# Kernel optimization log

Hardware: AMD Instinct MI355X
Metric: run time of the kernel (lower is better)

## Reference

```python
import jax, jax.numpy as jnp
import numpy as np

B, T, M, D, H, DK, DV = 2, 1024, 1024, 1024, 16, 64, 64
R = 2 * T + M  # number of relative positions required by rel_shift path


def setup_inputs() -> dict:
    key = jax.random.key(0)
    ks = jax.random.split(key, 11)
    s = 0.02
    return {
        "inputs": jax.random.normal(ks[0], (B, T, D), jnp.float32),
        "attention_mask": jnp.ones((B, T, M + T), jnp.float32),
        "positional_encodings": jax.random.normal(ks[1], (R, D), jnp.float32),
        "memory": jax.random.normal(ks[2], (B, M, D), jnp.float32),
        "Wq": jax.random.normal(ks[3], (D, H * DK), jnp.float32) * s,
        "Wk": jax.random.normal(ks[4], (D, H * DK), jnp.float32) * s,
        "Wv": jax.random.normal(ks[5], (D, H * DV), jnp.float32) * s,
        "Wr": jax.random.normal(ks[6], (D, H * DK), jnp.float32) * s,
        "r_w_bias": jax.random.normal(ks[7], (H, DK), jnp.float32) * s,
        "r_r_bias": jax.random.normal(ks[8], (H, DK), jnp.float32) * s,
        "W_out": jax.random.normal(ks[9], (H * DV, D), jnp.float32) * s,
    }


def _rel_shift(m, attention_length):
    # m: [T_q, T_q + L] -> [T_q, L], TXL relative shift via reshape/slice
    tq, total = m.shape
    x = m.reshape(total, tq)[1:].reshape(tq, total - 1)
    return x[:, :attention_length]


def reference(inputs, attention_mask, positional_encodings, memory,
              Wq, Wk, Wv, Wr, r_w_bias, r_r_bias, W_out):
    b, t, d = inputs.shape
    values = jnp.concatenate([memory, inputs], axis=1)  # [B, L, D]
    L = values.shape[1]
    q = (inputs @ Wq).reshape(b, t, H, DK)
    k = (values @ Wk).reshape(b, L, H, DK)
    v = (values @ Wv).reshape(b, L, H, DV)
    rk = (positional_encodings @ Wr).reshape(-1, H, DK)  # [R, H, DK]
    # content + relative logits (TXL)
    content = jnp.einsum('bthd,bThd->bhtT', q + r_w_bias, k)        # [B,H,T,L]
    rel = jnp.einsum('bthd,rhd->bhtr', q + r_r_bias, rk)            # [B,H,T,R]
    rel = jax.vmap(jax.vmap(lambda m: _rel_shift(m, L)))(rel)       # [B,H,T,L]
    logits = (content + rel) * (DK ** -0.5)
    masked = logits - (1.0 - attention_mask[:, None, :, :]) * 1e30
    w = jax.nn.softmax(masked, axis=-1)
    attn = jnp.einsum('bhtT,bThd->bthd', w, v)                      # [B,T,H,DV]
    return attn.reshape(b, t, H * DV) @ W_out
```

## Files before the change

### kernel.cpp

```cpp
#include <hip/hip_runtime.h>
#include <hip/hip_fp16.h>
#include <stdint.h>

#define Bz 2
#define Tq 1024
#define Mm 1024
#define Hh 16
#define Ll 2048
#define Rr 3072

typedef __attribute__((ext_vector_type(8))) short bf16x8;
typedef __attribute__((ext_vector_type(4))) float f32x4;

typedef __attribute__((address_space(3))) uint8_t lds_u8_t;
typedef __attribute__((address_space(1))) uint8_t glb_u8_t;

__device__ __forceinline__ void gl2lds16(const void* g, void* l) {
  __builtin_amdgcn_global_load_lds((const glb_u8_t*)g, (lds_u8_t*)l, 16, 0, 0);
}

__device__ __forceinline__ unsigned short f2bf(float f) {
  unsigned int u = __builtin_bit_cast(unsigned int, f);
  u = u + 0x7fffu + ((u >> 16) & 1u);
  return (unsigned short)(u >> 16);
}
__device__ __forceinline__ float b2f(unsigned short s) {
  unsigned int u = ((unsigned int)s) << 16;
  return __builtin_bit_cast(float, u);
}
__device__ __forceinline__ unsigned int cvt_pk_bf16(float lo, float hi) {
  unsigned int r;
  asm volatile("v_cvt_pk_bf16_f32 %0, %1, %2" : "=v"(r) : "v"(lo), "v"(hi));
  return r;
}

__global__ __launch_bounds__(256) void k_prep2(
    const float* __restrict__ x, const float* __restrict__ mem,
    const float* __restrict__ pos,
    const float* __restrict__ w0, const float* __restrict__ w1,
    const float* __restrict__ w2, const float* __restrict__ w3,
    const float* __restrict__ w4,
    unsigned short* __restrict__ vin, unsigned short* __restrict__ pb,
    unsigned short* __restrict__ t0, unsigned short* __restrict__ t1,
    unsigned short* __restrict__ t2, unsigned short* __restrict__ t3,
    unsigned short* __restrict__ t4) {
  __shared__ float tile[64][65];
  int bid = blockIdx.x;
  if (bid < 4096) {
    int idx = bid * 256 + threadIdx.x;
    int e = idx << 2;
    int row = e >> 10, col = e & 1023;
    int b = row >> 11, l = row & 2047;
    const float* s = (l < Mm) ? (mem + (((size_t)b * Mm + l) << 10) + col)
                              : (x + (((size_t)b * Tq + (l - Mm)) << 10) + col);
    float4 v = *(const float4*)s;
    ushort4 o;
    o.x = f2bf(v.x); o.y = f2bf(v.y); o.z = f2bf(v.z); o.w = f2bf(v.w);
    *(ushort4*)(vin + e) = o;
  } else if (bid < 7168) {
    int idx = (bid - 4096) * 256 + threadIdx.x;
    int e = idx << 2;
    float4 v = *(const float4*)(pos + e);
    ushort4 t;
    t.x = f2bf(v.x); t.y = f2bf(v.y); t.z = f2bf(v.z); t.w = f2bf(v.w);
    *(ushort4*)(pb + e) = t;
  } else {
    int r3 = bid - 7168;
    int mz = r3 >> 8, rem = r3 & 255;
    const float* W;
    unsigned short* WT;
    switch (mz) {
      case 0: W = w0; WT = t0; break;
      case 1: W = w1; WT = t1; break;
      case 2: W = w2; WT = t2; break;
      case 3: W = w3; WT = t3; break;
      default: W = w4; WT = t4; break;
    }
    int k0 = (rem >> 4) * 64, n0 = (rem & 15) * 64;
    int tid = threadIdx.x;
    int rr = tid >> 4, c4 = (tid & 15) * 4;
#pragma unroll
    for (int it = 0; it < 4; ++it) {
      int r = rr + it * 16;
      float4 v = *(const float4*)(W + (size_t)(k0 + r) * 1024 + n0 + c4);
      tile[r][c4] = v.x; tile[r][c4 + 1] = v.y;
      tile[r][c4 + 2] = v.z; tile[r][c4 + 3] = v.w;
    }
    __syncthreads();
#pragma unroll
    for (int it = 0; it < 4; ++it) {
      int n = rr + it * 16;
      ushort4 o;
      o.x = f2bf(tile[c4 + 0][n]); o.y = f2bf(tile[c4 + 1][n]);
      o.z = f2bf(tile[c4 + 2][n]); o.w = f2bf(tile[c4 + 3][n]);
      *(ushort4*)(WT + (size_t)(n0 + n) * 1024 + k0 + c4) = o;
    }
  }
}

template <int RMAP>
__device__ __forceinline__ void gemm_pipe(const unsigned short* __restrict__ A,
                                          const unsigned short* __restrict__ Bt,
                                          int m0, int n0, unsigned short* As,
                                          unsigned short* Bs, f32x4 acc[4][4]) {
  const int tid = threadIdx.x;
  const int w = tid >> 6, lane = tid & 63;
  const int quad = lane >> 4, li = lane & 15;
  const int wr = w >> 1, wc = w & 1;
  f32x4 z = {0.f, 0.f, 0.f, 0.f};
#pragma unroll
  for (int mi = 0; mi < 4; ++mi)
#pragma unroll
    for (int ni = 0; ni < 4; ++ni) acc[mi][ni] = z;

  const int rs = lane >> 2;
  const int cs = lane & 3;

#pragma unroll
  for (int s = 0; s < 2; ++s) {
    int i = w * 2 + s;
    int r = i * 16 + rs;
    int c = cs ^ ((r >> 1) & 3);
    int ar = m0 + r;
    if (RMAP) ar = ar + 1024 + (ar & 1024);
    gl2lds16(A + (size_t)ar * 1024 + c * 8, (char*)As + i * 1024);
    gl2lds16(Bt + (size_t)(n0 + r) * 1024 + c * 8, (char*)Bs + i * 1024);
  }

  for (int k0 = 0; k0 < 1024; k0 += 32) {
    const int bo = ((k0 >> 5) & 1) * 8192;
    const int no = bo ^ 8192;
    __builtin_amdgcn_s_waitcnt(0x0F70);
    __syncthreads();
    if (k0 + 32 < 1024) {
#pragma unroll
      for (int s = 0; s < 2; ++s) {
        int i = w * 2 + s;
        int r = i * 16 + rs;
        int c = cs ^ ((r >> 1) & 3);
        int ar = m0 + r;
        if (RMAP) ar = ar + 1024 + (ar & 1024);
        gl2lds16(A + (size_t)ar * 1024 + k0 + 32 + c * 8,
                 (char*)As + no + i * 1024);
        gl2lds16(Bt + (size_t)(n0 + r) * 1024 + k0 + 32 + c * 8,
                 (char*)Bs + no + i * 1024);
      }
    }
    bf16x8 af[4], bfr[4];
#pragma unroll
    for (int mi = 0; mi < 4; ++mi) {
      int r = wr * 64 + mi * 16 + li;
      int ch = quad ^ ((r >> 1) & 3);
      af[mi] = *(const bf16x8*)((const char*)As + bo + r * 64 + ch * 16);
    }
#pragma unroll
    for (int ni = 0; ni < 4; ++ni) {
      int r = wc * 64 + ni * 16 + li;
      int ch = quad ^ ((r >> 1) & 3);
      bfr[ni] = *(const bf16x8*)((const char*)Bs + bo + r * 64 + ch * 16);
    }
#pragma unroll
    for (int mi = 0; mi < 4; ++mi)
#pragma unroll
      for (int ni = 0; ni < 4; ++ni)
        acc[mi][ni] = __builtin_amdgcn_mfma_f32_16x16x32_bf16(
            af[mi], bfr[ni], acc[mi][ni], 0, 0, 0);
  }
}

__global__ __launch_bounds__(256) void k_proj(
    const unsigned short* __restrict__ Vin, const unsigned short* __restrict__ Pb,
    const unsigned short* __restrict__ WqT, const unsigned short* __restrict__ WkT,
    const unsigned short* __restrict__ WvT, const unsigned short* __restrict__ WrT,
    unsigned short* __restrict__ qb, unsigned short* __restrict__ kb,
    unsigned short* __restrict__ vtb, unsigned short* __restrict__ rkb) {
  __shared__ unsigned short As[2 * 128 * 32];
  __shared__ unsigned short Bs[2 * 128 * 32];
  const int t = blockIdx.x;
  const int tid = threadIdx.x, w = tid >> 6, lane = tid & 63;
  const int quad = lane >> 4, li = lane & 15, wr = w >> 1, wc = w & 1;
  f32x4 acc[4][4];

  if (t < 256) {
    int m0 = (t >> 3) * 128, n0 = (t & 7) * 128;
    gemm_pipe<0>(Vin, WkT, m0, n0, As, Bs, acc);
#pragma unroll
    for (int mi = 0; mi < 4; ++mi)
#pragma unroll
      for (int ni = 0; ni < 4; ++ni)
#pragma unroll
        for (int reg = 0; reg < 4; ++reg) {
          int rrow = m0 + wr * 64 + mi * 16 + quad * 4 + reg;
          int cc = n0 + wc * 64 + ni * 16 + li;
          kb[(size_t)rrow * 1024 + cc] = f2bf(acc[mi][ni][reg]);
        }
  } else if (t < 512) {
    int tt = t - 256;
    int m0 = (tt >> 3) * 128, n0 = (tt & 7) * 128;
    gemm_pipe<0>(Vin, WvT, m0, n0, As, Bs, acc);
    unsigned short* T = As;
    int b = m0 >> 11, l0b = m0 & 2047;
    int rr2 = tid >> 2, q2 = tid & 3;
#pragma unroll
    for (int p = 0; p < 2; ++p) {
      __syncthreads();
      if (wc == p) {
#pragma unroll
        for (int mi = 0; mi < 4; ++mi)
#pragma unroll
          for (int ni = 0; ni < 4; ++ni) {
            int ccl = ni * 16 + li;
            int ll = wr * 64 + mi * 16 + quad * 4;
            ushort4 o;
            o.x = f2bf(acc[mi][ni][0]); o.y = f2bf(acc[mi][ni][1]);
            o.z = f2bf(acc[mi][ni][2]); o.w = f2bf(acc[mi][ni][3]);
            *(ushort4*)(T + ccl * 128 + ll) = o;
          }
      }
      __syncthreads();
      const uint4* src = (const uint4*)(T + rr2 * 128 + q2 * 32);
      uint4 v0 = src[0], v1 = src[1], v2 = src[2], v3 = src[3];
      uint4* dp = (uint4*)(vtb +
          ((size_t)(b * 1024 + n0 + p * 64 + rr2)) * Ll + l0b + q2 * 32);
      dp[0] = v0; dp[1] = v1; dp[2] = v2; dp[3] = v3;
    }
  } else if (t < 640) {
    int tt = t - 512;
    int m0 = (tt >> 3) * 128, n0 = (tt & 7) * 128;
    gemm_pipe<1>(Vin, WqT, m0, n0, As, Bs, acc);
#pragma unroll
    for (int mi = 0; mi < 4; ++mi)
#pragma unroll
      for (int ni = 0; ni < 4; ++ni)
#pragma unroll
        for (int reg = 0; reg < 4; ++reg) {
          int rrow = m0 + wr * 64 + mi * 16 + quad * 4 + reg;
          int cc = n0 + wc * 64 + ni * 16 + li;
          qb[(size_t)rrow * 1024 + cc] = f2bf(acc[mi][ni][reg]);
        }
  } else {
    int tt = t - 640;
    int m0 = (tt >> 3) * 128, n0 = (tt & 7) * 128;
    gemm_pipe<0>(Pb, WrT, m0, n0, As, Bs, acc);
#pragma unroll
    for (int mi = 0; mi < 4; ++mi)
#pragma unroll
      for (int ni = 0; ni < 4; ++ni)
#pragma unroll
        for (int reg = 0; reg < 4; ++reg) {
          int rrow = m0 + wr * 64 + mi * 16 + quad * 4 + reg;
          int cc = n0 + wc * 64 + ni * 16 + li;
          rkb[(size_t)rrow * 1024 + cc] = f2bf(acc[mi][ni][reg]);
        }
  }
}

__global__ __launch_bounds__(256) void k_gemm_out64(
    const unsigned short* __restrict__ attnb, const unsigned short* __restrict__ WoT,
    float* __restrict__ out) {
  __shared__ unsigned short As[2 * 64 * 32];
  __shared__ unsigned short Bs[2 * 64 * 32];
  int m0 = blockIdx.x * 64, n0 = blockIdx.y * 64;
  const int tid = threadIdx.x, w = tid >> 6, lane = tid & 63;
  const int quad = lane >> 4, li = lane & 15, wr = w >> 1, wc = w & 1;
  f32x4 z = {0.f, 0.f, 0.f, 0.f};
  f32x4 acc[2][2];
#pragma unroll
  for (int mi = 0; mi < 2; ++mi)
#pragma unroll
    for (int ni = 0; ni < 2; ++ni) acc[mi][ni] = z;
  const int rs = lane >> 2, cs = lane & 3;

  {
    int r = w * 16 + rs;
    int c = cs ^ ((r >> 1) & 3);
    gl2lds16(attnb + (size_t)(m0 + r) * 1024 + c * 8, (char*)As + w * 1024);
    gl2lds16(WoT + (size_t)(n0 + r) * 1024 + c * 8, (char*)Bs + w * 1024);
  }

  for (int k0 = 0; k0 < 1024; k0 += 32) {
    const int bo = ((k0 >> 5) & 1) * 4096;
    __builtin_amdgcn_s_waitcnt(0x0F70);
    __syncthreads();
    if (k0 + 32 < 1024) {
      int r = w * 16 + rs;
      int c = cs ^ ((r >> 1) & 3);
      gl2lds16(attnb + (size_t)(m0 + r) * 1024 + k0 + 32 + c * 8,
               (char*)As + (bo ^ 4096) + w * 1024);
      gl2lds16(WoT + (size_t)(n0 + r) * 1024 + k0 + 32 + c * 8,
               (char*)Bs + (bo ^ 4096) + w * 1024);
    }
    bf16x8 af[2], bfr[2];
#pragma unroll
    for (int mi = 0; mi < 2; ++mi) {
      int r = wr * 32 + mi * 16 + li;
      int ch = quad ^ ((r >> 1) & 3);
      af[mi] = *(const bf16x8*)((const char*)As + bo + r * 64 + ch * 16);
    }
#pragma unroll
    for (int ni = 0; ni < 2; ++ni) {
      int r = wc * 32 + ni * 16 + li;
      int ch = quad ^ ((r >> 1) & 3);
      bfr[ni] = *(const bf16x8*)((const char*)Bs + bo + r * 64 + ch * 16);
    }
#pragma unroll
    for (int mi = 0; mi < 2; ++mi)
#pragma unroll
      for (int ni = 0; ni < 2; ++ni)
        acc[mi][ni] = __builtin_amdgcn_mfma_f32_16x16x32_bf16(
            af[mi], bfr[ni], acc[mi][ni], 0, 0, 0);
  }
#pragma unroll
  for (int mi = 0; mi < 2; ++mi)
#pragma unroll
    for (int ni = 0; ni < 2; ++ni)
#pragma unroll
      for (int reg = 0; reg < 4; ++reg) {
        int rrow = m0 + wr * 32 + mi * 16 + quad * 4 + reg;
        int cc = n0 + wc * 32 + ni * 16 + li;
        out[(size_t)rrow * 1024 + cc] = acc[mi][ni][reg];
      }
}

__global__ __launch_bounds__(512, 4) void k_attn(
    const unsigned short* __restrict__ qb, const float* __restrict__ rwb,
    const float* __restrict__ rrb,
    const unsigned short* __restrict__ kb, const unsigned short* __restrict__ vt,
    const unsigned short* __restrict__ rkb, const float* __restrict__ maskf,
    unsigned short* __restrict__ attnb) {
  __shared__ __align__(16) uint8_t lds[75776];

  const int tid = threadIdx.x;
  const int w = tid >> 6, lane = tid & 63;
  const int quad = lane >> 4, li = lane & 15;
  const int wq = w & 3, grp = w >> 2;
  const int srow = lane >> 3, scs = lane & 7;
  const int flat = blockIdx.x + 16 * blockIdx.y + 256 * blockIdx.z;
  const int qt = (flat >> 3) & 15;
  const int g = 4 * (flat & 7) + (flat >> 7);
  const int h = g & 15, b = g >> 4;
  const int t0blk = qt * 64;
  const int t0w = t0blk + wq * 16;
  const int rboff = 48 - 16 * wq;
  const int rbase0 = Tq - t0blk - 63;
  const int jbase = grp * 1024;

  unsigned short* KS = (unsigned short*)(lds + grp * 8192);
  unsigned short* VS = (unsigned short*)(lds + 16384 + grp * 8192);
  unsigned short* RS = (unsigned short*)(lds + 32768 + grp * 16384);
  unsigned short* pw = (unsigned short*)(lds + 65536 + w * 1280);
  float* red = (float*)(lds + 32768);

  const unsigned short* kbase = kb + ((size_t)(b * Ll + jbase) * Hh + h) * 64;
  const unsigned short* vbase = vt + ((size_t)((b * Hh + h) * 64)) * Ll + jbase;
  const unsigned short* rkbase = rkb + (size_t)h * 64;
  const float* mrowf = maskf + ((size_t)(b * Tq + t0w + li)) * Ll + jbase;

  bf16x8 aqw[2], aqr[2];
  {
    const unsigned short* p1 = qb + ((size_t)((b * Tq + t0w + li) * Hh + h)) * 64;
#pragma unroll
    for (int ks = 0; ks < 2; ++ks) {
      bf16x8 qf = *(const bf16x8*)(p1 + ks * 32 + quad * 8);
      const float* wp = rwb + h * 64 + ks * 32 + quad * 8;
      const float* rp = rrb + h * 64 + ks * 32 + quad * 8;
      float4 w0 = *(const float4*)wp, w1 = *(const float4*)(wp + 4);
      float4 r0 = *(const float4*)rp, r1 = *(const float4*)(rp + 4);
      float wv[8] = {w0.x, w0.y, w0.z, w0.w, w1.x, w1.y, w1.z, w1.w};
      float rv[8] = {r0.x, r0.y, r0.z, r0.w, r1.x, r1.y, r1.z, r1.w};
#pragma unroll
      for (int i2 = 0; i2 < 8; ++i2) {
        float qv = b2f((unsigned short)qf[i2]);
        aqw[ks][i2] = (short)f2bf(qv + wv[i2]);
        aqr[ks][i2] = (short)f2bf(qv + rv[i2]);
      }
    }
  }

  f32x4 z = {0.f, 0.f, 0.f, 0.f};
  f32x4 o[4];
  o[0] = z; o[1] = z; o[2] = z; o[3] = z;
  f32x4 ol = z;
  float nmf[8] = {0.f, 0.f, 0.f, 0.f, 0.f, 0.f, 0.f, 0.f};

  const float SC = 0.125f * 1.4426950408889634f;
  const float BIGM = 1.442695e30f;
  const short oneb = 0x3F80;
  const bf16x8 onesf = {oneb, oneb, oneb, oneb, oneb, oneb, oneb, oneb};

  int srcl[4];
#pragma unroll
  for (int reg = 0; reg < 4; ++reg) {
    int row = quad * 4 + reg;
    srcl[reg] = (lane & 48) + ((li + row + 1) & 15);
  }

  auto finish = [&](const unsigned short* VsP, const float (&mv)[8]) {
    bf16x8 sv = *(const bf16x8*)(pw + li * 40 + quad * 8);
    float p[8];
#pragma unroll
    for (int i2 = 0; i2 < 8; ++i2) {
      float sf = __half2float(__builtin_bit_cast(__half, (unsigned short)sv[i2]));
      float mvneg = fmaf(mv[i2], BIGM, -BIGM);
      p[i2] = exp2f(fmaf(sf, SC, mvneg));
    }
    int4 pk;
    pk.x = (int)cvt_pk_bf16(p[0], p[1]);
    pk.y = (int)cvt_pk_bf16(p[2], p[3]);
    pk.z = (int)cvt_pk_bf16(p[4], p[5]);
    pk.w = (int)cvt_pk_bf16(p[6], p[7]);
    bf16x8 apv = __builtin_bit_cast(bf16x8, pk);
    __builtin_amdgcn_s_setprio(1);
    ol = __builtin_amdgcn_mfma_f32_16x16x32_bf16(apv, onesf, ol, 0, 0, 0);
#pragma unroll
    for (int nt = 0; nt < 4; ++nt) {
      int dv = nt * 16 + li;
      int ch = quad ^ ((dv >> 1) & 3);
      bf16x8 vf = *(const bf16x8*)(VsP + dv * 32 + ch * 8);
      o[nt] = __builtin_amdgcn_mfma_f32_16x16x32_bf16(apv, vf, o[nt], 0, 0, 0);
    }
    __builtin_amdgcn_s_setprio(0);
  };

#pragma unroll
  for (int pass = 0; pass < 3; ++pass) {
    int u = pass * 32 + wq * 8 + srow;
    int gr = rbase0 + jbase + u;
    if (gr > Rr - 1) gr = Rr - 1;
    int c = scs ^ srow;
    gl2lds16(rkbase + (size_t)gr * 1024 + c * 8, RS + (pass * 32 + wq * 8) * 64);
  }
  {
    int r = wq * 8 + srow;
    int c = scs ^ srow;
    gl2lds16(kbase + (size_t)r * 1024 + c * 8, KS + wq * 512);
  }

  for (int jt = 0; jt < 32; ++jt) {
    const int jloc = jt * 32;
    __builtin_amdgcn_s_waitcnt(0x0F70);
    __syncthreads();
    if (jt < 31) {
      {
        int r = wq * 8 + srow;
        int c = scs ^ srow;
        gl2lds16(kbase + (size_t)(jloc + 32 + r) * 1024 + c * 8,
                 KS + (((jt + 1) & 1) * 2048) + wq * 512);
      }
      {
        int u = jloc + 96 + wq * 8 + srow;
        int gr = rbase0 + jbase + u;
        if (gr > Rr - 1) gr = Rr - 1;
        int c = scs ^ srow;
        gl2lds16(rkbase + (size_t)gr * 1024 + c * 8,
                 RS + ((jloc + 96 + wq * 8) & 127) * 64);
      }
    }
    {
      int dv = wq * 16 + (lane >> 2);
      int c = (lane & 3) ^ ((dv >> 1) & 3);
      gl2lds16(vbase + (size_t)dv * Ll + jloc + c * 8,
               VS + ((jt & 1) * 2048) + wq * 512);
    }
    asm volatile("" ::: "memory");
    const unsigned short* KsC = KS + (jt & 1) * 2048;
    f32x4 sc[2];
    sc[0] = z; sc[1] = z;
    __builtin_amdgcn_s_setprio(1);
#pragma unroll
    for (int ks = 0; ks < 2; ++ks)
#pragma unroll
      for (int nt = 0; nt < 2; ++nt) {
        int j = nt * 16 + li;
        int ch = (ks * 4 + quad) ^ (j & 7);
        bf16x8 kf = *(const bf16x8*)(KsC + j * 64 + ch * 8);
        sc[nt] = __builtin_amdgcn_mfma_f32_16x16x32_bf16(aqw[ks], kf, sc[nt], 0, 0, 0);
      }
    f32x4 bd[3];
    bd[0] = z; bd[1] = z; bd[2] = z;
#pragma unroll
    for (int ks = 0; ks < 2; ++ks)
#pragma unroll
      for (int nt = 0; nt < 3; ++nt) {
        int pr = (rboff + nt * 16 + li + jloc) & 127;
        int ch = (ks * 4 + quad) ^ (pr & 7);
        bf16x8 rf = *(const bf16x8*)(RS + pr * 64 + ch * 8);
        bd[nt] = __builtin_amdgcn_mfma_f32_16x16x32_bf16(aqr[ks], rf, bd[nt], 0, 0, 0);
      }
    __builtin_amdgcn_s_setprio(0);
    if (jt > 0) finish(VS + ((jt - 1) & 1) * 2048, nmf);
    {
      float4 m0 = *(const float4*)(mrowf + jloc + quad * 8);
      float4 m1 = *(const float4*)(mrowf + jloc + quad * 8 + 4);
      nmf[0] = m0.x; nmf[1] = m0.y; nmf[2] = m0.z; nmf[3] = m0.w;
      nmf[4] = m1.x; nmf[5] = m1.y; nmf[6] = m1.z; nmf[7] = m1.w;
    }
    float rot[2][4];
#pragma unroll
    for (int nt = 0; nt < 2; ++nt)
#pragma unroll
      for (int reg = 0; reg < 4; ++reg)
        rot[nt][reg] = __shfl(sc[nt][reg], srcl[reg], 64);
#pragma unroll
    for (int nt = 0; nt < 3; ++nt)
#pragma unroll
      for (int reg = 0; reg < 4; ++reg) {
        int row = quad * 4 + reg;
        int jj = nt * 16 + li + row - 15;
        int nthi = (nt > 1) ? 0 : nt;
        int ntlo = (nt == 0) ? 0 : (nt - 1);
        float val = ((li + row) >= 15) ? rot[nthi][reg] : rot[ntlo][reg];
        float s = val + bd[nt][reg];
        if ((unsigned)jj < 32u)
          pw[row * 40 + jj] = __builtin_bit_cast(unsigned short, __float2half(s));
      }
  }
  __builtin_amdgcn_s_waitcnt(0x0F70);
  __syncthreads();
  finish(VS + 2048, nmf);

  if (grp == 1) {
    float* rp = red + (size_t)(wq * 64 + lane) * 20;
#pragma unroll
    for (int nt = 0; nt < 4; ++nt)
#pragma unroll
      for (int reg = 0; reg < 4; ++reg) rp[nt * 4 + reg] = o[nt][reg];
#pragma unroll
    for (int reg = 0; reg < 4; ++reg) rp[16 + reg] = ol[reg];
  }
  __syncthreads();
  if (grp == 0) {
    const float* rp = red + (size_t)(wq * 64 + lane) * 20;
    float inv[4];
#pragma unroll
    for (int reg = 0; reg < 4; ++reg) inv[reg] = 1.0f / (ol[reg] + rp[16 + reg]);
#pragma unroll
    for (int nt = 0; nt < 4; ++nt)
#pragma unroll
      for (int reg = 0; reg < 4; ++reg) {
        int trow = t0w + quad * 4 + reg;
        float val = (o[nt][reg] + rp[nt * 4 + reg]) * inv[reg];
        attnb[((size_t)(b * Tq + trow)) * 1024 + h * 64 + nt * 16 + li] = f2bf(val);
      }
  }
}

extern "C" void kernel_launch(void* const* d_in, const int* in_sizes, int n_in,
                              void* d_out, int out_size, void* d_ws, size_t ws_size,
                              hipStream_t stream) {
  const float* x = (const float*)d_in[0];
  const float* mask = (const float*)d_in[1];
  const float* pos = (const float*)d_in[2];
  const float* mem = (const float*)d_in[3];
  const float* Wq = (const float*)d_in[4];
  const float* Wk = (const float*)d_in[5];
  const float* Wv = (const float*)d_in[6];
  const float* Wr = (const float*)d_in[7];
  const float* rwb = (const float*)d_in[8];
  const float* rrb = (const float*)d_in[9];
  const float* Wo = (const float*)d_in[10];
  float* out = (float*)d_out;

  uint8_t* ws = (uint8_t*)d_ws;
  const size_t MB = 1024 * 1024;
  unsigned short* Vinb = (unsigned short*)(ws + 0);
  unsigned short* WqT = (unsigned short*)(ws + 8 * MB);
  unsigned short* WkT = (unsigned short*)(ws + 10 * MB);
  unsigned short* WvT = (unsigned short*)(ws + 12 * MB);
  unsigned short* WrT = (unsigned short*)(ws + 14 * MB);
  unsigned short* WoT = (unsigned short*)(ws + 16 * MB);
  unsigned short* Pb = (unsigned short*)(ws + 18 * MB);
  unsigned short* qb = (unsigned short*)(ws + 24 * MB);
  unsigned short* kb = (unsigned short*)(ws + 32 * MB);
  unsigned short* vtb = (unsigned short*)(ws + 40 * MB);
  unsigned short* rkb = (unsigned short*)(ws + 48 * MB);
  unsigned short* attnb = (unsigned short*)(ws + 19 * MB);

  hipLaunchKernelGGL(k_prep2, dim3(8448), dim3(256), 0, stream,
                     x, mem, pos, Wq, Wk, Wv, Wr, Wo,
                     Vinb, Pb, WqT, WkT, WvT, WrT, WoT);
  hipLaunchKernelGGL(k_proj, dim3(832), dim3(256), 0, stream,
                     Vinb, Pb, WqT, WkT, WvT, WrT, qb, kb, vtb, rkb);
  hipLaunchKernelGGL(k_attn, dim3(16, 16, 2), dim3(512), 0, stream,
                     qb, rwb, rrb, kb, vtb, rkb, mask, attnb);
  hipLaunchKernelGGL(k_gemm_out64, dim3(32, 16), dim3(256), 0, stream,
                     attnb, WoT, out);
}
```

Before: 268.6 us.

## Remap projection tile order for XCD locality and drop LDS transpose for V

Block indices in the fused projection kernel are remapped so that consecutive blocks (likely spread round-robin across the 8 XCDs) share the same row band. This is meant to improve L2 reuse of A and B tiles. The V-projection epilogue no longer stages a transpose through LDS with two barriers. Each wave instead writes ushort4 fragments straight into the transposed layout. That removes the syncs and LDS traffic but gives narrower, more scattered global stores.

```diff
diff --git a/kernel.cpp b/kernel.cpp
--- a/kernel.cpp
+++ b/kernel.cpp
@@ -182,7 +182,8 @@
   f32x4 acc[4][4];
 
   if (t < 256) {
-    int m0 = (t >> 3) * 128, n0 = (t & 7) * 128;
+    int a = t & 7, n = (t >> 3) & 7, c = t >> 6;
+    int m0 = (4 * a + c) * 128, n0 = n * 128;
     gemm_pipe<0>(Vin, WkT, m0, n0, As, Bs, acc);
 #pragma unroll
     for (int mi = 0; mi < 4; ++mi)
@@ -195,38 +196,26 @@
           kb[(size_t)rrow * 1024 + cc] = f2bf(acc[mi][ni][reg]);
         }
   } else if (t < 512) {
-    int tt = t - 256;
-    int m0 = (tt >> 3) * 128, n0 = (tt & 7) * 128;
+    int f = t - 256;
+    int a = f & 7, n = (f >> 3) & 7, c = f >> 6;
+    int m0 = (4 * a + c) * 128, n0 = n * 128;
     gemm_pipe<0>(Vin, WvT, m0, n0, As, Bs, acc);
-    unsigned short* T = As;
-    int b = m0 >> 11, l0b = m0 & 2047;
-    int rr2 = tid >> 2, q2 = tid & 3;
-#pragma unroll
-    for (int p = 0; p < 2; ++p) {
-      __syncthreads();
-      if (wc == p) {
-#pragma unroll
-        for (int mi = 0; mi < 4; ++mi)
-#pragma unroll
-          for (int ni = 0; ni < 4; ++ni) {
-            int ccl = ni * 16 + li;
-            int ll = wr * 64 + mi * 16 + quad * 4;
-            ushort4 o;
-            o.x = f2bf(acc[mi][ni][0]); o.y = f2bf(acc[mi][ni][1]);
-            o.z = f2bf(acc[mi][ni][2]); o.w = f2bf(acc[mi][ni][3]);
-            *(ushort4*)(T + ccl * 128 + ll) = o;
-          }
-      }
-      __syncthreads();
-      const uint4* src = (const uint4*)(T + rr2 * 128 + q2 * 32);
-      uint4 v0 = src[0], v1 = src[1], v2 = src[2], v3 = src[3];
-      uint4* dp = (uint4*)(vtb +
-          ((size_t)(b * 1024 + n0 + p * 64 + rr2)) * Ll + l0b + q2 * 32);
-      dp[0] = v0; dp[1] = v1; dp[2] = v2; dp[3] = v3;
-    }
+#pragma unroll
+    for (int mi = 0; mi < 4; ++mi)
+#pragma unroll
+      for (int ni = 0; ni < 4; ++ni) {
+        int r0 = m0 + wr * 64 + mi * 16 + quad * 4;
+        int b = r0 >> 11, l0 = r0 & 2047;
+        int cc = n0 + wc * 64 + ni * 16 + li;
+        ushort4 o;
+        o.x = f2bf(acc[mi][ni][0]); o.y = f2bf(acc[mi][ni][1]);
+        o.z = f2bf(acc[mi][ni][2]); o.w = f2bf(acc[mi][ni][3]);
+        *(ushort4*)(vtb + ((size_t)(b * 1024 + cc)) * Ll + l0) = o;
+      }
   } else if (t < 640) {
-    int tt = t - 512;
-    int m0 = (tt >> 3) * 128, n0 = (tt & 7) * 128;
+    int f = t - 512;
+    int a = f & 7, n = (f >> 3) & 7, c = f >> 6;
+    int m0 = (2 * a + c) * 128, n0 = n * 128;
     gemm_pipe<1>(Vin, WqT, m0, n0, As, Bs, acc);
 #pragma unroll
     for (int mi = 0; mi < 4; ++mi)
@@ -239,8 +228,9 @@
           qb[(size_t)rrow * 1024 + cc] = f2bf(acc[mi][ni][reg]);
         }
   } else {
-    int tt = t - 640;
-    int m0 = (tt >> 3) * 128, n0 = (tt & 7) * 128;
+    int f = t - 640;
+    int a = f & 7, n = (f >> 3) & 7, c = f >> 6;
+    int m0 = (3 * a + c) * 128, n0 = n * 128;
     gemm_pipe<0>(Pb, WrT, m0, n0, As, Bs, acc);
 #pragma unroll
     for (int mi = 0; mi < 4; ++mi)
```

Result: faster. 239.7 us (-10.8%).
